# Performance work log

Hardware: AMD Instinct MI355X
Metric: run time of the kernel (lower is better)

Reference implementation:

```python
import jax, jax.numpy as jnp
import numpy as np

NUM_HEADS = 8
LN_EPS = 1e-5


def setup_inputs() -> dict:
    key = jax.random.key(0)
    ks = jax.random.split(key, 12)
    N, H, G = 100000, 512, 256
    s = 1.0 / np.sqrt(H)
    return {
        "x": jax.random.normal(ks[0], (N, H), dtype=jnp.float32),
        "batch": jnp.sort(jax.random.randint(ks[1], (N,), 0, G)),
        "query": jax.random.normal(ks[2], (H,), dtype=jnp.float32),
        "k_w": jax.random.uniform(ks[3], (H, H), minval=-s, maxval=s, dtype=jnp.float32),
        "k_b": jax.random.uniform(ks[4], (H,), minval=-s, maxval=s, dtype=jnp.float32),
        "v_w": jax.random.uniform(ks[5], (H, H), minval=-s, maxval=s, dtype=jnp.float32),
        "v_b": jax.random.uniform(ks[6], (H,), minval=-s, maxval=s, dtype=jnp.float32),
        "o_w": jax.random.uniform(ks[7], (H, H), minval=-s, maxval=s, dtype=jnp.float32),
        "o_b": jax.random.uniform(ks[8], (H,), minval=-s, maxval=s, dtype=jnp.float32),
        "ln_g": jnp.ones((H,), dtype=jnp.float32),
        "ln_b": jnp.zeros((H,), dtype=jnp.float32),
        "num_graphs": 256,
    }


def reference(x, batch, query, k_w, k_b, v_w, v_b, o_w, o_b, ln_g, ln_b, num_graphs):
    N, H = x.shape
    nh = NUM_HEADS
    hd = H // nh
    # projections (torch Linear: x @ W.T + b)
    k = (x @ k_w.T + k_b).reshape(N, nh, hd)
    v = (x @ v_w.T + v_b).reshape(N, nh, hd)
    q = query.reshape(nh, hd)
    # per-node, per-head attention logits against the shared graph query
    s = jnp.einsum("nhd,hd->nh", k, q) / np.float32(np.sqrt(hd))  # [N, nh]
    # segment softmax over nodes of each graph (stable via segment max)
    s_max = jax.ops.segment_max(s, batch, num_segments=num_graphs)  # [G, nh]
    w = jnp.exp(s - s_max[batch])  # [N, nh]
    denom = jax.ops.segment_sum(w, batch, num_segments=num_graphs)  # [G, nh]
    numer = jax.ops.segment_sum(w[:, :, None] * v, batch, num_segments=num_graphs)  # [G, nh, hd]
    attended = numer / jnp.where(denom > 0, denom, 1.0)[:, :, None]  # zeros for empty graphs
    out = attended.reshape(num_graphs, H)
    out = out @ o_w.T + o_b
    # layer norm over last dim
    mu = out.mean(-1, keepdims=True)
    var = out.var(-1, keepdims=True)
    out = (out - mu) / jnp.sqrt(var + LN_EPS) * ln_g + ln_b
    return out
```

## Files before the change

kernel.cpp:

```cpp
#include <hip/hip_runtime.h>
#include <math.h>

#define H 512
#define NH 8
#define NG 256
#define SPLIT 4

#define WS_QK   0
#define WS_SB   4096
#define WS_SEG  4352
#define WS_VWT  8192
#define WS_OWT  270336
#define WS_TP   532480
#define WS_DP   4726784


__global__ __launch_bounds__(256) void k_seg(const int* __restrict__ batch, int N,
                                             int* __restrict__ seg) {
  int g = blockIdx.x * 256 + threadIdx.x;
  if (g > NG) return;
  int lo = 0, hi = N;
  while (lo < hi) { int mid = (lo + hi) >> 1; if (batch[mid] < g) lo = mid + 1; else hi = mid; }
  seg[g] = lo;
}

__global__ __launch_bounds__(256) void k_qk(const float* __restrict__ k_w,
                                            const float* __restrict__ k_b,
                                            const float* __restrict__ query,
                                            float* __restrict__ qk, float* __restrict__ sb) {
  int gt = blockIdx.x * 256 + threadIdx.x;
  int h = gt >> 9, j = gt & 511;
  float a = 0.f;
#pragma unroll 8
  for (int d = 0; d < 64; ++d)
    a = fmaf(k_w[(size_t)(h * 64 + d) * H + j], query[h * 64 + d], a);
  qk[j * 8 + h] = a;
  if (gt < 8) {
    float s = 0.f;
    for (int d = 0; d < 64; ++d) s = fmaf(k_b[gt * 64 + d], query[gt * 64 + d], s);
    sb[gt] = s;
  }
}

__global__ __launch_bounds__(256) void k_transpose(const float* __restrict__ vw,
                                                   const float* __restrict__ ow,
                                                   float* __restrict__ vwt,
                                                   float* __restrict__ owt) {
  __shared__ float tile[32][33];
  const float* in  = (blockIdx.y == 0) ? vw  : ow;
  float*       out = (blockIdx.y == 0) ? vwt : owt;
  int b = blockIdx.x;
  int bx = b & 15, by = b >> 4;
  int tx = threadIdx.x & 31, ty = threadIdx.x >> 5;
#pragma unroll
  for (int k = 0; k < 4; ++k)
    tile[ty + 8 * k][tx] = in[(size_t)(by * 32 + ty + 8 * k) * H + bx * 32 + tx];
  __syncthreads();
#pragma unroll
  for (int k = 0; k < 4; ++k)
    out[(size_t)(bx * 32 + ty + 8 * k) * H + by * 32 + tx] = tile[tx][ty + 8 * k];
}


__device__ __forceinline__ float dpp_add(float v, int t) { return v + __int_as_float(t); }

__device__ __forceinline__ float wave_allreduce(float v) {
  v = dpp_add(v, __builtin_amdgcn_update_dpp(0, __float_as_int(v), 0x128, 0xf, 0xf, false));
  v = dpp_add(v, __builtin_amdgcn_update_dpp(0, __float_as_int(v), 0x124, 0xf, 0xf, false));
  v = dpp_add(v, __builtin_amdgcn_update_dpp(0, __float_as_int(v), 0x122, 0xf, 0xf, false));
  v = dpp_add(v, __builtin_amdgcn_update_dpp(0, __float_as_int(v), 0x121, 0xf, 0xf, false));
  v += __shfl_xor(v, 16, 64);
  v += __shfl_xor(v, 32, 64);
  return v;
}

__global__ __launch_bounds__(256, 2) void k_main(
    const float* __restrict__ x, const float* __restrict__ qk, const float* __restrict__ sb,
    const int* __restrict__ seg, float* __restrict__ T_part, float* __restrict__ den_part) {
  const int g = blockIdx.x >> 2, p = blockIdx.x & (SPLIT - 1);
  const int s0 = seg[g], e0 = seg[g + 1], len = e0 - s0;
  const int na = s0 + (len * p) / SPLIT;
  const int nb = s0 + (len * (p + 1)) / SPLIT;
  const int lane = threadIdx.x & 63, wid = threadIdx.x >> 6;

  float qk_r[8][8];
#pragma unroll
  for (int ci = 0; ci < 8; ++ci) {
    int j = (ci < 4) ? (4 * lane + ci) : (256 + 4 * lane + ci - 4);
    const float4* row = (const float4*)(qk + j * 8);
    float4 q0 = row[0], q1 = row[1];
    qk_r[ci][0] = q0.x; qk_r[ci][1] = q0.y; qk_r[ci][2] = q0.z; qk_r[ci][3] = q0.w;
    qk_r[ci][4] = q1.x; qk_r[ci][5] = q1.y; qk_r[ci][6] = q1.z; qk_r[ci][7] = q1.w;
  }
  float sbr[8];
#pragma unroll
  for (int h = 0; h < 8; ++h) sbr[h] = sb[h];

  float T_r[8][8];
  float den[8];
#pragma unroll
  for (int h = 0; h < 8; ++h) {
    den[h] = 0.f;
#pragma unroll
    for (int ci = 0; ci < 8; ++ci) T_r[h][ci] = 0.f;
  }

  const float4* x4 = (const float4*)x;
  int n = na + wid;
  float4 xa, xb;
  if (n < nb) { size_t base = (size_t)n * 128 + lane; xa = x4[base]; xb = x4[base + 64]; }
  while (n < nb) {
    int n2 = n + 4;
    float4 ya, yb;
    if (n2 < nb) { size_t b2 = (size_t)n2 * 128 + lane; ya = x4[b2]; yb = x4[b2 + 64]; }

    float xv[8] = {xa.x, xa.y, xa.z, xa.w, xb.x, xb.y, xb.z, xb.w};
    float pp[8] = {0.f, 0.f, 0.f, 0.f, 0.f, 0.f, 0.f, 0.f};
#pragma unroll
    for (int ci = 0; ci < 8; ++ci)
#pragma unroll
      for (int h = 0; h < 8; ++h) pp[h] = fmaf(xv[ci], qk_r[ci][h], pp[h]);

    float w[8];
#pragma unroll
    for (int h = 0; h < 8; ++h) {
      float s = wave_allreduce(pp[h]);
      w[h] = __expf((s + sbr[h]) * 0.125f);
      den[h] += w[h];
    }
#pragma unroll
    for (int h = 0; h < 8; ++h)
#pragma unroll
      for (int ci = 0; ci < 8; ++ci) T_r[h][ci] = fmaf(w[h], xv[ci], T_r[h][ci]);

    xa = ya; xb = yb; n = n2;
  }

  __shared__ float T_lds[8][512];
  __shared__ float den_lds[4][8];
  for (int wv = 0; wv < 4; ++wv) {
    if (wid == wv) {
#pragma unroll
      for (int h = 0; h < 8; ++h) {
        float4 v0 = make_float4(T_r[h][0], T_r[h][1], T_r[h][2], T_r[h][3]);
        float4 v1 = make_float4(T_r[h][4], T_r[h][5], T_r[h][6], T_r[h][7]);
        float4* d0 = (float4*)&T_lds[h][4 * lane];
        float4* d1 = (float4*)&T_lds[h][256 + 4 * lane];
        if (wv == 0) { *d0 = v0; *d1 = v1; }
        else {
          float4 o0 = *d0, o1 = *d1;
          o0.x += v0.x; o0.y += v0.y; o0.z += v0.z; o0.w += v0.w;
          o1.x += v1.x; o1.y += v1.y; o1.z += v1.z; o1.w += v1.w;
          *d0 = o0; *d1 = o1;
        }
      }
      if (lane == 0) {
#pragma unroll
        for (int h = 0; h < 8; ++h) den_lds[wv][h] = den[h];
      }
    }
    __syncthreads();
  }
  const int gp = blockIdx.x;
  float4* Tp4 = (float4*)(T_part + (size_t)gp * (NH * H));
  const float4* Tl4 = (const float4*)T_lds;
  for (int k = threadIdx.x; k < NH * H / 4; k += 256) Tp4[k] = Tl4[k];
  if (threadIdx.x < 8) {
    float d = den_lds[0][threadIdx.x] + den_lds[1][threadIdx.x] +
              den_lds[2][threadIdx.x] + den_lds[3][threadIdx.x];
    den_part[gp * 8 + threadIdx.x] = d;
  }
}


__global__ __launch_bounds__(512, 1) void k_epi(
    const float* __restrict__ T_part, const float* __restrict__ den_part,
    const float* __restrict__ vwt, const float* __restrict__ vb,
    const float* __restrict__ owt, const float* __restrict__ ob,
    const float* __restrict__ lng, const float* __restrict__ lnb,
    float* __restrict__ out) {
  const int g = blockIdx.x;
  const int t = threadIdx.x;
  __shared__ float Tl[NH * H];
  __shared__ float att[H];
  __shared__ float den_s[8], dinv_s[8];
  __shared__ float red1[8], red2[8];

  {
    const float4* tp = (const float4*)(T_part + (size_t)g * SPLIT * (NH * H));
    float4* tl4 = (float4*)Tl;
    for (int k = t; k < NH * H / 4; k += 512) {
      float4 acc = tp[k];
#pragma unroll
      for (int p = 1; p < SPLIT; ++p) {
        float4 v = tp[p * (NH * H / 4) + k];
        acc.x += v.x; acc.y += v.y; acc.z += v.z; acc.w += v.w;
      }
      tl4[k] = acc;
    }
    if (t < 8) {
      float d = 0.f;
#pragma unroll
      for (int p = 0; p < SPLIT; ++p) d += den_part[(g * SPLIT + p) * 8 + t];
      den_s[t] = d;
      dinv_s[t] = (d > 0.f) ? 1.f / d : 1.f;
    }
  }
  __syncthreads();

  {
    const int h = t >> 6;
    const float* Th = Tl + h * H;
    float acc = 0.f;
#pragma unroll 8
    for (int j = 0; j < H; ++j) acc = fmaf(Th[j], vwt[(size_t)j * H + t], acc);
    att[t] = (acc + den_s[h] * vb[t]) * dinv_s[h];
  }
  __syncthreads();

  float o = ob[t];
#pragma unroll 8
  for (int k = 0; k < H; ++k) o = fmaf(att[k], owt[(size_t)k * H + t], o);

  float r1 = o, r2 = o * o;
#pragma unroll
  for (int m = 1; m < 64; m <<= 1) { r1 += __shfl_xor(r1, m, 64); r2 += __shfl_xor(r2, m, 64); }
  if ((t & 63) == 0) { red1[t >> 6] = r1; red2[t >> 6] = r2; }
  __syncthreads();
  float S1 = 0.f, S2 = 0.f;
#pragma unroll
  for (int w = 0; w < 8; ++w) { S1 += red1[w]; S2 += red2[w]; }
  float mu = S1 * (1.f / 512.f);
  float var = S2 * (1.f / 512.f) - mu * mu;
  float rstd = rsqrtf(var + 1e-5f);
  out[(size_t)g * H + t] = (o - mu) * rstd * lng[t] + lnb[t];
}


extern "C" void kernel_launch(void* const* d_in, const int* in_sizes, int n_in,
                              void* d_out, int out_size, void* d_ws, size_t ws_size,
                              hipStream_t stream) {
  const float* x     = (const float*)d_in[0];
  const int*   batch = (const int*)d_in[1];
  const float* query = (const float*)d_in[2];
  const float* k_w   = (const float*)d_in[3];
  const float* k_b   = (const float*)d_in[4];
  const float* v_w   = (const float*)d_in[5];
  const float* v_b   = (const float*)d_in[6];
  const float* o_w   = (const float*)d_in[7];
  const float* o_b   = (const float*)d_in[8];
  const float* ln_g  = (const float*)d_in[9];
  const float* ln_b  = (const float*)d_in[10];
  const int N = in_sizes[0] / H;

  float* ws  = (float*)d_ws;
  float* qk  = ws + WS_QK;
  float* sb  = ws + WS_SB;
  int*   seg = (int*)(ws + WS_SEG);
  float* vwt = ws + WS_VWT;
  float* owt = ws + WS_OWT;
  float* Tp  = ws + WS_TP;
  float* dp  = ws + WS_DP;

  hipLaunchKernelGGL(k_seg, dim3(2), dim3(256), 0, stream, batch, N, seg);
  hipLaunchKernelGGL(k_qk, dim3(16), dim3(256), 0, stream, k_w, k_b, query, qk, sb);
  hipLaunchKernelGGL(k_transpose, dim3(256, 2), dim3(256), 0, stream, v_w, o_w, vwt, owt);
  hipLaunchKernelGGL(k_main, dim3(NG * SPLIT), dim3(256), 0, stream, x, qk, sb, seg, Tp, dp);
  hipLaunchKernelGGL(k_epi, dim3(NG), dim3(512), 0, stream, Tp, dp, vwt, v_b, owt, o_b,
                     ln_g, ln_b, (float*)d_out);
}
```

Measured before the change: 389.7 us.

## Merge setup kernels, batch DPP reductions, deepen prefetch, two graphs per epilogue block

Three small setup kernels become one launch, dispatched on block index. The 1/sqrt(hd) scale is folded into qk and sb. The main loop now prefetches x two rows ahead and does the eight per-head wave reductions in interleaved row_shr/row_bcast DPP steps with a readlane, replacing the shfl_xor stages. The epilogue handles two graphs per block so each vwt/owt weight load is reused twice, halving weight traffic at the cost of more LDS and fewer blocks.

```diff
diff --git a/kernel.cpp b/kernel.cpp
--- a/kernel.cpp
+++ b/kernel.cpp
@@ -15,64 +15,54 @@
 #define WS_DP   4726784
 
 
-__global__ __launch_bounds__(256) void k_seg(const int* __restrict__ batch, int N,
-                                             int* __restrict__ seg) {
-  int g = blockIdx.x * 256 + threadIdx.x;
-  if (g > NG) return;
-  int lo = 0, hi = N;
-  while (lo < hi) { int mid = (lo + hi) >> 1; if (batch[mid] < g) lo = mid + 1; else hi = mid; }
-  seg[g] = lo;
-}
-
-__global__ __launch_bounds__(256) void k_qk(const float* __restrict__ k_w,
-                                            const float* __restrict__ k_b,
-                                            const float* __restrict__ query,
-                                            float* __restrict__ qk, float* __restrict__ sb) {
-  int gt = blockIdx.x * 256 + threadIdx.x;
-  int h = gt >> 9, j = gt & 511;
-  float a = 0.f;
+__global__ __launch_bounds__(256) void k_setup(
+    const int* __restrict__ batch, int N, int* __restrict__ seg,
+    const float* __restrict__ k_w, const float* __restrict__ k_b,
+    const float* __restrict__ query, float* __restrict__ qk, float* __restrict__ sb,
+    const float* __restrict__ vw, const float* __restrict__ ow,
+    float* __restrict__ vwt, float* __restrict__ owt) {
+  __shared__ float tile[32][33];
+  const int b = blockIdx.x;
+  if (b < 2) {
+    int g = b * 256 + threadIdx.x;
+    if (g > NG) return;
+    int lo = 0, hi = N;
+    while (lo < hi) { int mid = (lo + hi) >> 1; if (batch[mid] < g) lo = mid + 1; else hi = mid; }
+    seg[g] = lo;
+  } else if (b < 18) {
+    int gt = (b - 2) * 256 + threadIdx.x;
+    int h = gt >> 9, j = gt & 511;
+    float a = 0.f;
 #pragma unroll 8
-  for (int d = 0; d < 64; ++d)
-    a = fmaf(k_w[(size_t)(h * 64 + d) * H + j], query[h * 64 + d], a);
-  qk[j * 8 + h] = a;
-  if (gt < 8) {
-    float s = 0.f;
-    for (int d = 0; d < 64; ++d) s = fmaf(k_b[gt * 64 + d], query[gt * 64 + d], s);
-    sb[gt] = s;
-  }
-}
-
-__global__ __launch_bounds__(256) void k_transpose(const float* __restrict__ vw,
-                                                   const float* __restrict__ ow,
-                                                   float* __restrict__ vwt,
-                                                   float* __restrict__ owt) {
-  __shared__ float tile[32][33];
-  const float* in  = (blockIdx.y == 0) ? vw  : ow;
-  float*       out = (blockIdx.y == 0) ? vwt : owt;
-  int b = blockIdx.x;
-  int bx = b & 15, by = b >> 4;
-  int tx = threadIdx.x & 31, ty = threadIdx.x >> 5;
-#pragma unroll
-  for (int k = 0; k < 4; ++k)
-    tile[ty + 8 * k][tx] = in[(size_t)(by * 32 + ty + 8 * k) * H + bx * 32 + tx];
-  __syncthreads();
-#pragma unroll
-  for (int k = 0; k < 4; ++k)
-    out[(size_t)(bx * 32 + ty + 8 * k) * H + by * 32 + tx] = tile[tx][ty + 8 * k];
-}
-
-
-__device__ __forceinline__ float dpp_add(float v, int t) { return v + __int_as_float(t); }
-
-__device__ __forceinline__ float wave_allreduce(float v) {
-  v = dpp_add(v, __builtin_amdgcn_update_dpp(0, __float_as_int(v), 0x128, 0xf, 0xf, false));
-  v = dpp_add(v, __builtin_amdgcn_update_dpp(0, __float_as_int(v), 0x124, 0xf, 0xf, false));
-  v = dpp_add(v, __builtin_amdgcn_update_dpp(0, __float_as_int(v), 0x122, 0xf, 0xf, false));
-  v = dpp_add(v, __builtin_amdgcn_update_dpp(0, __float_as_int(v), 0x121, 0xf, 0xf, false));
-  v += __shfl_xor(v, 16, 64);
-  v += __shfl_xor(v, 32, 64);
-  return v;
-}
+    for (int d = 0; d < 64; ++d)
+      a = fmaf(k_w[(size_t)(h * 64 + d) * H + j], query[h * 64 + d], a);
+    qk[j * 8 + h] = a * 0.125f;
+    if (gt < 8) {
+      float s = 0.f;
+      for (int d = 0; d < 64; ++d) s = fmaf(k_b[gt * 64 + d], query[gt * 64 + d], s);
+      sb[gt] = s * 0.125f;
+    }
+  } else {
+    int bb = b - 18;
+    const float* in  = (bb < 256) ? vw  : ow;
+    float*       out = (bb < 256) ? vwt : owt;
+    int tidx = bb & 255;
+    int bx = tidx & 15, by = tidx >> 4;
+    int tx = threadIdx.x & 31, ty = threadIdx.x >> 5;
+#pragma unroll
+    for (int k = 0; k < 4; ++k)
+      tile[ty + 8 * k][tx] = in[(size_t)(by * 32 + ty + 8 * k) * H + bx * 32 + tx];
+    __syncthreads();
+#pragma unroll
+    for (int k = 0; k < 4; ++k)
+      out[(size_t)(bx * 32 + ty + 8 * k) * H + by * 32 + tx] = tile[tx][ty + 8 * k];
+  }
+}
+
+
+#define DPP_ADD(v, ctrl, rmask)                                                   \
+  v += __int_as_float(__builtin_amdgcn_update_dpp(0, __float_as_int(v), ctrl,     \
+                                                  rmask, 0xf, true))
 
 __global__ __launch_bounds__(256, 2) void k_main(
     const float* __restrict__ x, const float* __restrict__ qk, const float* __restrict__ sb,
@@ -107,25 +97,39 @@
 
   const float4* x4 = (const float4*)x;
   int n = na + wid;
-  float4 xa, xb;
-  if (n < nb) { size_t base = (size_t)n * 128 + lane; xa = x4[base]; xb = x4[base + 64]; }
-  while (n < nb) {
-    int n2 = n + 4;
-    float4 ya, yb;
-    if (n2 < nb) { size_t b2 = (size_t)n2 * 128 + lane; ya = x4[b2]; yb = x4[b2 + 64]; }
-
-    float xv[8] = {xa.x, xa.y, xa.z, xa.w, xb.x, xb.y, xb.z, xb.w};
+  float4 b0a, b0b, b1a, b1b;
+  if (n < nb)     { size_t a = (size_t)n * 128 + lane;       b0a = x4[a]; b0b = x4[a + 64]; }
+  if (n + 4 < nb) { size_t a = (size_t)(n + 4) * 128 + lane; b1a = x4[a]; b1b = x4[a + 64]; }
+
+  for (; n < nb; n += 4) {
+    float4 b2a, b2b;
+    if (n + 8 < nb) { size_t a = (size_t)(n + 8) * 128 + lane; b2a = x4[a]; b2b = x4[a + 64]; }
+
+    float xv[8] = {b0a.x, b0a.y, b0a.z, b0a.w, b0b.x, b0b.y, b0b.z, b0b.w};
     float pp[8] = {0.f, 0.f, 0.f, 0.f, 0.f, 0.f, 0.f, 0.f};
 #pragma unroll
     for (int ci = 0; ci < 8; ++ci)
 #pragma unroll
       for (int h = 0; h < 8; ++h) pp[h] = fmaf(xv[ci], qk_r[ci][h], pp[h]);
 
+#pragma unroll
+    for (int h = 0; h < 8; ++h) DPP_ADD(pp[h], 0x111, 0xf);
+#pragma unroll
+    for (int h = 0; h < 8; ++h) DPP_ADD(pp[h], 0x112, 0xf);
+#pragma unroll
+    for (int h = 0; h < 8; ++h) DPP_ADD(pp[h], 0x114, 0xf);
+#pragma unroll
+    for (int h = 0; h < 8; ++h) DPP_ADD(pp[h], 0x118, 0xf);
+#pragma unroll
+    for (int h = 0; h < 8; ++h) DPP_ADD(pp[h], 0x142, 0xa);
+#pragma unroll
+    for (int h = 0; h < 8; ++h) DPP_ADD(pp[h], 0x143, 0xc);
+
     float w[8];
 #pragma unroll
     for (int h = 0; h < 8; ++h) {
-      float s = wave_allreduce(pp[h]);
-      w[h] = __expf((s + sbr[h]) * 0.125f);
+      float s = __int_as_float(__builtin_amdgcn_readlane(__float_as_int(pp[h]), 63));
+      w[h] = __expf(s + sbr[h]);
       den[h] += w[h];
     }
 #pragma unroll
@@ -133,7 +137,7 @@
 #pragma unroll
       for (int ci = 0; ci < 8; ++ci) T_r[h][ci] = fmaf(w[h], xv[ci], T_r[h][ci]);
 
-    xa = ya; xb = yb; n = n2;
+    b0a = b1a; b0b = b1b; b1a = b2a; b1b = b2b;
   }
 
   __shared__ float T_lds[8][512];
@@ -173,22 +177,23 @@
 }
 
 
-__global__ __launch_bounds__(512, 1) void k_epi(
+__global__ __launch_bounds__(512) void k_epi(
     const float* __restrict__ T_part, const float* __restrict__ den_part,
     const float* __restrict__ vwt, const float* __restrict__ vb,
     const float* __restrict__ owt, const float* __restrict__ ob,
     const float* __restrict__ lng, const float* __restrict__ lnb,
     float* __restrict__ out) {
-  const int g = blockIdx.x;
+  const int g0 = blockIdx.x * 2;
   const int t = threadIdx.x;
-  __shared__ float Tl[NH * H];
-  __shared__ float att[H];
-  __shared__ float den_s[8], dinv_s[8];
-  __shared__ float red1[8], red2[8];
-
-  {
-    const float4* tp = (const float4*)(T_part + (size_t)g * SPLIT * (NH * H));
-    float4* tl4 = (float4*)Tl;
+  __shared__ float Tl[2][NH * H];
+  __shared__ float att[2][H];
+  __shared__ float den_s[2][8], dinv_s[2][8];
+  __shared__ float red[2][2][8];
+
+#pragma unroll
+  for (int gi = 0; gi < 2; ++gi) {
+    const float4* tp = (const float4*)(T_part + (size_t)(g0 + gi) * SPLIT * (NH * H));
+    float4* tl4 = (float4*)Tl[gi];
     for (int k = t; k < NH * H / 4; k += 512) {
       float4 acc = tp[k];
 #pragma unroll
@@ -198,42 +203,65 @@
       }
       tl4[k] = acc;
     }
-    if (t < 8) {
-      float d = 0.f;
-#pragma unroll
-      for (int p = 0; p < SPLIT; ++p) d += den_part[(g * SPLIT + p) * 8 + t];
-      den_s[t] = d;
-      dinv_s[t] = (d > 0.f) ? 1.f / d : 1.f;
-    }
+  }
+  if (t < 16) {
+    int gi = t >> 3, h = t & 7;
+    float d = 0.f;
+#pragma unroll
+    for (int p = 0; p < SPLIT; ++p) d += den_part[((g0 + gi) * SPLIT + p) * 8 + h];
+    den_s[gi][h] = d;
+    dinv_s[gi][h] = (d > 0.f) ? 1.f / d : 1.f;
   }
   __syncthreads();
 
   {
     const int h = t >> 6;
-    const float* Th = Tl + h * H;
-    float acc = 0.f;
+    const float* T0 = &Tl[0][h * H];
+    const float* T1 = &Tl[1][h * H];
+    float a0 = 0.f, a1 = 0.f;
 #pragma unroll 8
-    for (int j = 0; j < H; ++j) acc = fmaf(Th[j], vwt[(size_t)j * H + t], acc);
-    att[t] = (acc + den_s[h] * vb[t]) * dinv_s[h];
+    for (int j = 0; j < H; ++j) {
+      float wv_ = vwt[(size_t)j * H + t];
+      a0 = fmaf(T0[j], wv_, a0);
+      a1 = fmaf(T1[j], wv_, a1);
+    }
+    att[0][t] = (a0 + den_s[0][h] * vb[t]) * dinv_s[0][h];
+    att[1][t] = (a1 + den_s[1][h] * vb[t]) * dinv_s[1][h];
   }
   __syncthreads();
 
-  float o = ob[t];
+  float o0 = ob[t], o1 = o0;
 #pragma unroll 8
-  for (int k = 0; k < H; ++k) o = fmaf(att[k], owt[(size_t)k * H + t], o);
-
-  float r1 = o, r2 = o * o;
-#pragma unroll
-  for (int m = 1; m < 64; m <<= 1) { r1 += __shfl_xor(r1, m, 64); r2 += __shfl_xor(r2, m, 64); }
-  if ((t & 63) == 0) { red1[t >> 6] = r1; red2[t >> 6] = r2; }
+  for (int k = 0; k < H; ++k) {
+    float w_ = owt[(size_t)k * H + t];
+    o0 = fmaf(att[0][k], w_, o0);
+    o1 = fmaf(att[1][k], w_, o1);
+  }
+
+  float r10 = o0, r20 = o0 * o0, r11 = o1, r21 = o1 * o1;
+#pragma unroll
+  for (int m = 1; m < 64; m <<= 1) {
+    r10 += __shfl_xor(r10, m, 64); r20 += __shfl_xor(r20, m, 64);
+    r11 += __shfl_xor(r11, m, 64); r21 += __shfl_xor(r21, m, 64);
+  }
+  if ((t & 63) == 0) {
+    red[0][0][t >> 6] = r10; red[0][1][t >> 6] = r20;
+    red[1][0][t >> 6] = r11; red[1][1][t >> 6] = r21;
+  }
   __syncthreads();
-  float S1 = 0.f, S2 = 0.f;
-#pragma unroll
-  for (int w = 0; w < 8; ++w) { S1 += red1[w]; S2 += red2[w]; }
-  float mu = S1 * (1.f / 512.f);
-  float var = S2 * (1.f / 512.f) - mu * mu;
-  float rstd = rsqrtf(var + 1e-5f);
-  out[(size_t)g * H + t] = (o - mu) * rstd * lng[t] + lnb[t];
+  float S10 = 0.f, S20 = 0.f, S11 = 0.f, S21 = 0.f;
+#pragma unroll
+  for (int w = 0; w < 8; ++w) {
+    S10 += red[0][0][w]; S20 += red[0][1][w];
+    S11 += red[1][0][w]; S21 += red[1][1][w];
+  }
+  float mu0 = S10 * (1.f / 512.f), mu1 = S11 * (1.f / 512.f);
+  float var0 = S20 * (1.f / 512.f) - mu0 * mu0;
+  float var1 = S21 * (1.f / 512.f) - mu1 * mu1;
+  float rs0 = rsqrtf(var0 + 1e-5f), rs1 = rsqrtf(var1 + 1e-5f);
+  float gg = lng[t], bb = lnb[t];
+  out[(size_t)g0 * H + t]       = (o0 - mu0) * rs0 * gg + bb;
+  out[(size_t)(g0 + 1) * H + t] = (o1 - mu1) * rs1 * gg + bb;
 }
 
 
@@ -262,10 +290,9 @@
   float* Tp  = ws + WS_TP;
   float* dp  = ws + WS_DP;
 
-  hipLaunchKernelGGL(k_seg, dim3(2), dim3(256), 0, stream, batch, N, seg);
-  hipLaunchKernelGGL(k_qk, dim3(16), dim3(256), 0, stream, k_w, k_b, query, qk, sb);
-  hipLaunchKernelGGL(k_transpose, dim3(256, 2), dim3(256), 0, stream, v_w, o_w, vwt, owt);
+  hipLaunchKernelGGL(k_setup, dim3(530), dim3(256), 0, stream,
+                     batch, N, seg, k_w, k_b, query, qk, sb, v_w, o_w, vwt, owt);
   hipLaunchKernelGGL(k_main, dim3(NG * SPLIT), dim3(256), 0, stream, x, qk, sb, seg, Tp, dp);
-  hipLaunchKernelGGL(k_epi, dim3(NG), dim3(512), 0, stream, Tp, dp, vwt, v_b, owt, o_b,
+  hipLaunchKernelGGL(k_epi, dim3(NG / 2), dim3(512), 0, stream, Tp, dp, vwt, v_b, owt, o_b,
                      ln_g, ln_b, (float*)d_out);
 }
```

New measurement: 373.2 us. 4.2% less time.
